# Optimization experiments

Hardware: AMD Instinct MI355X
Metric: run time of the kernel (lower is better)

The kernel has to match this reference:

```python
import jax, jax.numpy as jnp
import numpy as np

N_NODES = 100000
N_EDGES = 1600000
NFEAT, NHID, NCLASS = 128, 64, 40
GN_GROUPS = 32  # min(32, nhid)
GN_EPS = 1e-5
ODE_STEPS = 4   # fixed-step RK4 over t in [0, 1] (stands in for adaptive dopri5)


def setup_inputs() -> dict:
    key = jax.random.key(0)
    ks = jax.random.split(key, 10)
    return {
        "x": jax.random.normal(ks[0], (N_NODES, NFEAT), dtype=jnp.float32),
        "src": jax.random.randint(ks[1], (N_EDGES,), 0, N_NODES),
        "tgt": jax.random.randint(ks[2], (N_EDGES,), 0, N_NODES),
        "mtgt_w": jax.random.uniform(ks[3], (N_EDGES,), dtype=jnp.float32),
        "W0": jax.random.normal(ks[4], (NFEAT, NHID), dtype=jnp.float32) * (1.0 / np.sqrt(NFEAT)),
        "b0": jnp.zeros((NHID,), jnp.float32),
        "gn_w": jnp.ones((NHID,), jnp.float32),
        "gn_b": jnp.zeros((NHID,), jnp.float32),
        "W1": jax.random.normal(ks[5], (NFEAT // 2 + 1, NHID), dtype=jnp.float32) * (1.0 / np.sqrt(NHID + 1)),
        "b1": jnp.zeros((NHID,), jnp.float32),
        "W2": jax.random.normal(ks[6], (NHID, NCLASS), dtype=jnp.float32) * (1.0 / np.sqrt(NHID)),
        "b2": jnp.zeros((NCLASS,), jnp.float32),
    }


def _gconv(h, W, b, src, tgt, mtgt_w, n_nodes):
    # linear transform, gather messages at src, scatter-sum into tgt weighted by Mtgt nonzeros
    s = h @ W + b                                   # [N, out]
    msg = mtgt_w[:, None] * s[src]                  # [E, out]
    return jax.ops.segment_sum(msg, tgt, num_segments=n_nodes)


def _groupnorm(h, gn_w, gn_b):
    n, c = h.shape
    g = h.reshape(n, GN_GROUPS, c // GN_GROUPS)
    mu = g.mean(axis=2, keepdims=True)
    var = g.var(axis=2, keepdims=True)
    g = (g - mu) * jax.lax.rsqrt(var + GN_EPS)
    return g.reshape(n, c) * gn_w + gn_b


def reference(x, src, tgt, mtgt_w, W0, b0, gn_w, gn_b, W1, b1, W2, b2):
    n = x.shape[0]
    # layer 0: GraphConvolution + relu (dropout is identity in eval mode)
    h = jax.nn.relu(_gconv(x, W0, b0, src, tgt, mtgt_w, n))

    # ODE block: dh/dt = relu(gconv(concat([t, groupnorm(h)], 1)))
    def f(t, h):
        hn = _groupnorm(h, gn_w, gn_b)
        tt = jnp.full((n, 1), t, dtype=h.dtype)
        return jax.nn.relu(_gconv(jnp.concatenate([tt, hn], axis=1), W1, b1, src, tgt, mtgt_w, n))

    dt = jnp.float32(1.0 / ODE_STEPS)
    ts = jnp.arange(ODE_STEPS, dtype=jnp.float32) * dt

    def rk4_step(h, t):
        k1 = f(t, h)
        k2 = f(t + dt / 2, h + dt / 2 * k1)
        k3 = f(t + dt / 2, h + dt / 2 * k2)
        k4 = f(t + dt, h + dt * k3)
        return h + dt / 6 * (k1 + 2 * k2 + 2 * k3 + k4), None

    h, _ = jax.lax.scan(rk4_step, h, ts)

    # final GraphConvolution + log_softmax
    out = _gconv(h, W2, b2, src, tgt, mtgt_w, n)
    return jax.nn.log_softmax(out, axis=1)
```

## Files before the change

kernel.cpp:

```cpp
#include <hip/hip_runtime.h>
#include <hip/hip_fp16.h>
#include <math.h>


constexpr int kN = 100000;
constexpr int kE = 1600000;
constexpr int kNPAD = 100352;
constexpr float kDT = 0.25f;
constexpr float kEPS = 1e-5f;

__device__ __forceinline__ float4 ld4(const float* p) { return *(const float4*)p; }
__device__ __forceinline__ void st4(float* p, float4 v) { *(float4*)p = v; }

__global__ void k_zero(int* cnt) {
  int i = blockIdx.x * 256 + threadIdx.x;
  if (i < kN) cnt[i] = 0;
}

__global__ void k_hist(const int* __restrict__ tgt, int* __restrict__ cnt) {
  int e = blockIdx.x * 256 + threadIdx.x;
  if (e < kE) atomicAdd(&cnt[tgt[e]], 1);
}

__global__ __launch_bounds__(256) void k_scan_a(const int* __restrict__ cnt,
                                                int* __restrict__ ptr,
                                                int* __restrict__ bsum) {
  int tid = threadIdx.x;
  int base = blockIdx.x * 1024;
  int i0 = base + tid * 4;
  int v[4];
#pragma unroll
  for (int t = 0; t < 4; ++t) v[t] = (i0 + t < kN) ? cnt[i0 + t] : 0;
  int ts = v[0] + v[1] + v[2] + v[3];
  int lane = tid & 63;
  int x = ts;
#pragma unroll
  for (int off = 1; off < 64; off <<= 1) {
    int y = __shfl_up(x, off);
    if (lane >= off) x += y;
  }
  __shared__ int wsum[4];
  if (lane == 63) wsum[tid >> 6] = x;
  __syncthreads();
  int woff = 0;
#pragma unroll
  for (int w = 0; w < 4; ++w)
    if (w < (tid >> 6)) woff += wsum[w];
  int o = woff + (x - ts);
#pragma unroll
  for (int t = 0; t < 4; ++t) {
    if (i0 + t < kN) ptr[i0 + t] = o;
    o += v[t];
  }
  if (tid == 255) bsum[blockIdx.x] = woff + x;
}

__global__ void k_scan_b(int* bsum, int nb) {
  int lane = threadIdx.x;
  int carry = 0;
  for (int b = 0; b < nb; b += 64) {
    int i = b + lane;
    int v = (i < nb) ? bsum[i] : 0;
    int x = v;
#pragma unroll
    for (int off = 1; off < 64; off <<= 1) {
      int y = __shfl_up(x, off);
      if (lane >= off) x += y;
    }
    if (i < nb) bsum[i] = carry + x - v;
    carry += __shfl(x, 63);
  }
}

__global__ void k_scan_c(const int* __restrict__ bsum, int* __restrict__ ptr,
                         int* __restrict__ runp) {
  int i = blockIdx.x * 256 + threadIdx.x;
  if (i < kN) {
    int v = ptr[i] + bsum[i >> 10];
    ptr[i] = v;
    runp[i] = v;
  }
  if (i == 0) ptr[kN] = kE;
}

__global__ void k_scatter(const int* __restrict__ src, const int* __restrict__ tgt,
                          const float* __restrict__ w, int* __restrict__ runp,
                          float2* __restrict__ meta) {
  int e = blockIdx.x * 256 + threadIdx.x;
  if (e < kE) {
    int t = tgt[e];
    int pos = atomicAdd(&runp[t], 1);
    meta[pos] = make_float2(__int_as_float(src[e]), w[e]);
  }
}

template <bool DSUM>
__device__ __forceinline__ void g_chunk4(const float2* __restrict__ meta,
                                         const float4* __restrict__ S4,
                                         int e, int rem, int slot, int fc,
                                         float4& acc, float& ds) {
  float2 m0 = meta[e + 0], m1 = meta[e + 1], m2 = meta[e + 2], m3 = meta[e + 3];
  int idx = slot == 1 ? __float_as_int(m1.x)
          : slot == 2 ? __float_as_int(m2.x)
          : slot == 3 ? __float_as_int(m3.x)
                      : __float_as_int(m0.x);
  float w = slot == 1 ? m1.y : slot == 2 ? m2.y : slot == 3 ? m3.y : m0.y;
  if (rem < 4) {
    bool ok = slot < rem;
    idx = ok ? idx : 0;
    w = ok ? w : 0.f;
  }
  float4 v = S4[idx * 16 + fc];
  acc.x += w * v.x; acc.y += w * v.y; acc.z += w * v.z; acc.w += w * v.w;
  if (DSUM) ds += w;
}

template <bool DSUM>
__device__ __forceinline__ float4 gather_row4(const float2* __restrict__ meta,
                                              const float4* __restrict__ S4,
                                              int e0, int e1, int slot, int fc,
                                              float& dsum) {
  float4 acc = make_float4(0.f, 0.f, 0.f, 0.f);
  float ds = 0.f;
  int e = e0;
  for (; e + 16 <= e1; e += 16) {
    g_chunk4<DSUM>(meta, S4, e + 0, 4, slot, fc, acc, ds);
    g_chunk4<DSUM>(meta, S4, e + 4, 4, slot, fc, acc, ds);
    g_chunk4<DSUM>(meta, S4, e + 8, 4, slot, fc, acc, ds);
    g_chunk4<DSUM>(meta, S4, e + 12, 4, slot, fc, acc, ds);
  }
  if (e + 8 <= e1) {
    g_chunk4<DSUM>(meta, S4, e + 0, 4, slot, fc, acc, ds);
    g_chunk4<DSUM>(meta, S4, e + 4, 4, slot, fc, acc, ds);
    e += 8;
  }
  if (e + 4 <= e1) {
    g_chunk4<DSUM>(meta, S4, e, 4, slot, fc, acc, ds);
    e += 4;
  }
  if (e < e1) g_chunk4<DSUM>(meta, S4, e, e1 - e, slot, fc, acc, ds);
  acc.x += __shfl_xor(acc.x, 16); acc.y += __shfl_xor(acc.y, 16);
  acc.z += __shfl_xor(acc.z, 16); acc.w += __shfl_xor(acc.w, 16);
  acc.x += __shfl_xor(acc.x, 32); acc.y += __shfl_xor(acc.y, 32);
  acc.z += __shfl_xor(acc.z, 32); acc.w += __shfl_xor(acc.w, 32);
  if (DSUM) {
    ds += __shfl_xor(ds, 16);
    ds += __shfl_xor(ds, 32);
    dsum = ds;
  }
  return acc;
}

__device__ __forceinline__ void g_chunk4h(const float2* __restrict__ meta,
                                          const uint2* __restrict__ Sh,
                                          int e, int rem, int slot, int fc,
                                          float4& acc) {
  float2 m0 = meta[e + 0], m1 = meta[e + 1], m2 = meta[e + 2], m3 = meta[e + 3];
  int idx = slot == 1 ? __float_as_int(m1.x)
          : slot == 2 ? __float_as_int(m2.x)
          : slot == 3 ? __float_as_int(m3.x)
                      : __float_as_int(m0.x);
  float w = slot == 1 ? m1.y : slot == 2 ? m2.y : slot == 3 ? m3.y : m0.y;
  if (rem < 4) {
    bool ok = slot < rem;
    idx = ok ? idx : 0;
    w = ok ? w : 0.f;
  }
  uint2 u = Sh[idx * 16 + fc];
  float2 f01 = __half22float2(*(const __half2*)&u.x);
  float2 f23 = __half22float2(*(const __half2*)&u.y);
  acc.x += w * f01.x; acc.y += w * f01.y;
  acc.z += w * f23.x; acc.w += w * f23.y;
}

__device__ __forceinline__ float4 gather_row4h(const float2* __restrict__ meta,
                                               const uint2* __restrict__ Sh,
                                               int e0, int e1, int slot, int fc) {
  float4 acc = make_float4(0.f, 0.f, 0.f, 0.f);
  int e = e0;
  for (; e + 16 <= e1; e += 16) {
    g_chunk4h(meta, Sh, e + 0, 4, slot, fc, acc);
    g_chunk4h(meta, Sh, e + 4, 4, slot, fc, acc);
    g_chunk4h(meta, Sh, e + 8, 4, slot, fc, acc);
    g_chunk4h(meta, Sh, e + 12, 4, slot, fc, acc);
  }
  if (e + 8 <= e1) {
    g_chunk4h(meta, Sh, e + 0, 4, slot, fc, acc);
    g_chunk4h(meta, Sh, e + 4, 4, slot, fc, acc);
    e += 8;
  }
  if (e + 4 <= e1) {
    g_chunk4h(meta, Sh, e, 4, slot, fc, acc);
    e += 4;
  }
  if (e < e1) g_chunk4h(meta, Sh, e, e1 - e, slot, fc, acc);
  acc.x += __shfl_xor(acc.x, 16); acc.y += __shfl_xor(acc.y, 16);
  acc.z += __shfl_xor(acc.z, 16); acc.w += __shfl_xor(acc.w, 16);
  acc.x += __shfl_xor(acc.x, 32); acc.y += __shfl_xor(acc.y, 32);
  acc.z += __shfl_xor(acc.z, 32); acc.w += __shfl_xor(acc.w, 32);
  return acc;
}

__device__ __forceinline__ void st_half4(unsigned short* p, float4 v) {
  __half2 a = __floats2half2_rn(v.x, v.y);
  __half2 b = __floats2half2_rn(v.z, v.w);
  uint2 u = make_uint2(*(unsigned*)&a, *(unsigned*)&b);
  *(uint2*)p = u;
}

__global__ __launch_bounds__(256) void k_spmm_l0(
    const int* __restrict__ ptr, const float2* __restrict__ meta,
    const float4* __restrict__ S4, float* __restrict__ h,
    unsigned short* __restrict__ hn, const float* __restrict__ gn_w,
    const float* __restrict__ gn_b, float* __restrict__ degw) {
  int wid = (blockIdx.x * 256 + threadIdx.x) >> 6;
  int lane = threadIdx.x & 63;
  if (wid >= kN) return;
  int slot = lane >> 4, fc = lane & 15;
  int e0 = __builtin_amdgcn_readfirstlane(ptr[wid]);
  int e1 = __builtin_amdgcn_readfirstlane(ptr[wid + 1]);
  float dsum = 0.f;
  float4 acc = gather_row4<true>(meta, S4, e0, e1, slot, fc, dsum);
  float4 hv = make_float4(fmaxf(acc.x, 0.f), fmaxf(acc.y, 0.f),
                          fmaxf(acc.z, 0.f), fmaxf(acc.w, 0.f));
  float dx = 0.5f * (hv.x - hv.y);
  float rx = dx * rsqrtf(dx * dx + kEPS);
  float dz = 0.5f * (hv.z - hv.w);
  float rz = dz * rsqrtf(dz * dz + kEPS);
  float4 gw = ld4(gn_w + fc * 4);
  float4 gb = ld4(gn_b + fc * 4);
  float4 o = make_float4(rx * gw.x + gb.x, -rx * gw.y + gb.y,
                         rz * gw.z + gb.z, -rz * gw.w + gb.w);
  if (slot == 0) {
    st4(h + wid * 64 + fc * 4, hv);
    st_half4(hn + wid * 64 + fc * 4, o);
    if (fc == 0) degw[wid] = dsum;
  }
}

__global__ __launch_bounds__(256) void k_spmm_ode(
    const int* __restrict__ ptr, const float2* __restrict__ meta,
    const uint2* __restrict__ Sh, float4* __restrict__ z4) {
  int wid = (blockIdx.x * 256 + threadIdx.x) >> 6;
  int lane = threadIdx.x & 63;
  if (wid >= kN) return;
  int slot = lane >> 4, fc = lane & 15;
  int e0 = __builtin_amdgcn_readfirstlane(ptr[wid]);
  int e1 = __builtin_amdgcn_readfirstlane(ptr[wid + 1]);
  float4 acc = gather_row4h(meta, Sh, e0, e1, slot, fc);
  if (slot == 0) z4[wid * 16 + fc] = acc;
}

__global__ __launch_bounds__(256) void k_gemm_stage(
    const float* __restrict__ z, const float* __restrict__ W1,
    const float* __restrict__ b1, const float* __restrict__ gn_w,
    const float* __restrict__ gn_b, const float* __restrict__ degw,
    float* __restrict__ h, float* __restrict__ kacc,
    unsigned short* __restrict__ hn, float t_s, float a_next, float coef,
    int init_acc, int is_stage3) {
  constexpr int NT = 128, ST = NT + 4, K = 64;
  __shared__ float Wl[K * 64];
  __shared__ float Zt[K * ST];
  const int tid = threadIdx.x;
  const int base = blockIdx.x * NT;
  const float* Wr = W1 + 64;
  for (int i = tid; i < K * 64; i += 256) Wl[i] = Wr[i];
  for (int idx = tid; idx < (K / 4) * NT; idx += 256) {
    int node = idx & (NT - 1);
    int k4 = idx >> 7;
    int g = base + node;
    float4 v = make_float4(0.f, 0.f, 0.f, 0.f);
    if (g < kN) v = ld4(z + (long)g * 64 + k4 * 4);
    int kk = k4 * 4;
    Zt[(kk + 0) * ST + node] = v.x;
    Zt[(kk + 1) * ST + node] = v.y;
    Zt[(kk + 2) * ST + node] = v.z;
    Zt[(kk + 3) * ST + node] = v.w;
  }
  __syncthreads();
  const int c0 = (tid & 15) * 4;
  const int n0 = (tid >> 4) * 8;
  float acc[8][4] = {};
#pragma unroll 8
  for (int j = 0; j < K; ++j) {
    float4 wv = ld4(Wl + j * 64 + c0);
    float4 za = ld4(Zt + j * ST + n0);
    float4 zb = ld4(Zt + j * ST + n0 + 4);
    float zv[8] = {za.x, za.y, za.z, za.w, zb.x, zb.y, zb.z, zb.w};
#pragma unroll
    for (int i = 0; i < 8; ++i) {
      acc[i][0] += zv[i] * wv.x;
      acc[i][1] += zv[i] * wv.y;
      acc[i][2] += zv[i] * wv.z;
      acc[i][3] += zv[i] * wv.w;
    }
  }
  float4 w0r = ld4(W1 + c0);
  float4 b1v = ld4(b1 + c0);
  float4 bias = make_float4(t_s * w0r.x + b1v.x, t_s * w0r.y + b1v.y,
                            t_s * w0r.z + b1v.z, t_s * w0r.w + b1v.w);
  float4 gw = ld4(gn_w + c0);
  float4 gb = ld4(gn_b + c0);
  const float c6 = kDT / 6.f;
#pragma unroll
  for (int i = 0; i < 8; ++i) {
    int g = base + n0 + i;
    if (g >= kN) break;
    float dg = degw[g];
    float4 kv = make_float4(fmaxf(acc[i][0] + dg * bias.x, 0.f),
                            fmaxf(acc[i][1] + dg * bias.y, 0.f),
                            fmaxf(acc[i][2] + dg * bias.z, 0.f),
                            fmaxf(acc[i][3] + dg * bias.w, 0.f));
    long o64 = (long)g * 64 + c0;
    float4 ka;
    if (init_acc) {
      ka = kv;
    } else {
      ka = ld4(kacc + o64);
      ka.x += coef * kv.x; ka.y += coef * kv.y;
      ka.z += coef * kv.z; ka.w += coef * kv.w;
    }
    if (!is_stage3) st4(kacc + o64, ka);
    float4 hv = ld4(h + o64);
    float4 y;
    if (is_stage3) {
      y = make_float4(hv.x + c6 * ka.x, hv.y + c6 * ka.y,
                      hv.z + c6 * ka.z, hv.w + c6 * ka.w);
      st4(h + o64, y);
    } else {
      y = make_float4(hv.x + a_next * kv.x, hv.y + a_next * kv.y,
                      hv.z + a_next * kv.z, hv.w + a_next * kv.w);
    }
    float dx = 0.5f * (y.x - y.y);
    float rx = dx * rsqrtf(dx * dx + kEPS);
    float dz = 0.5f * (y.z - y.w);
    float rz = dz * rsqrtf(dz * dz + kEPS);
    float4 o = make_float4(rx * gw.x + gb.x, -rx * gw.y + gb.y,
                           rz * gw.z + gb.z, -rz * gw.w + gb.w);
    st_half4(hn + o64, o);
  }
}

__global__ __launch_bounds__(256) void k_final(const int* __restrict__ ptr,
                                               const float2* __restrict__ meta,
                                               const float4* __restrict__ s2,
                                               float* __restrict__ out) {
  int wid = (blockIdx.x * 256 + threadIdx.x) >> 6;
  int lane = threadIdx.x & 63;
  if (wid >= kN) return;
  int slot = lane >> 4, fc = lane & 15;
  int e0 = __builtin_amdgcn_readfirstlane(ptr[wid]);
  int e1 = __builtin_amdgcn_readfirstlane(ptr[wid + 1]);
  float dum;
  float4 a = gather_row4<false>(meta, s2, e0, e1, slot, fc, dum);
  bool valid = fc < 10;
  float m = valid ? fmaxf(fmaxf(a.x, a.y), fmaxf(a.z, a.w)) : -INFINITY;
#pragma unroll
  for (int off = 1; off < 16; off <<= 1) m = fmaxf(m, __shfl_xor(m, off));
  float s = valid ? expf(a.x - m) + expf(a.y - m) + expf(a.z - m) + expf(a.w - m)
                  : 0.f;
#pragma unroll
  for (int off = 1; off < 16; off <<= 1) s += __shfl_xor(s, off);
  float lse = logf(s) + m;
  if (slot == 0 && valid)
    st4(out + (long)wid * 40 + fc * 4,
        make_float4(a.x - lse, a.y - lse, a.z - lse, a.w - lse));
}

template <int NCOL, int OST>
__global__ __launch_bounds__(256) void k_gemm64(const float* __restrict__ in,
                                                int in_stride,
                                                const float* __restrict__ W,
                                                const float* __restrict__ bias,
                                                float* __restrict__ out, int beta) {
  constexpr int NT = 128, ST = NT + 4, K = 64;
  __shared__ float Wl[K * 64];
  __shared__ float Zt[K * ST];
  const int tid = threadIdx.x;
  const int base = blockIdx.x * NT;
  for (int i = tid; i < K * 64; i += 256) {
    int j = i >> 6, c = i & 63;
    Wl[i] = (c < NCOL) ? W[j * NCOL + c] : 0.f;
  }
  for (int idx = tid; idx < (K / 4) * NT; idx += 256) {
    int node = idx & (NT - 1);
    int k4 = idx >> 7;
    int g = base + node;
    float4 v = make_float4(0.f, 0.f, 0.f, 0.f);
    if (g < kN) v = ld4(in + (long)g * in_stride + k4 * 4);
    int kk = k4 * 4;
    Zt[(kk + 0) * ST + node] = v.x;
    Zt[(kk + 1) * ST + node] = v.y;
    Zt[(kk + 2) * ST + node] = v.z;
    Zt[(kk + 3) * ST + node] = v.w;
  }
  __syncthreads();
  const int c0 = (tid & 15) * 4;
  const int n0 = (tid >> 4) * 8;
  float acc[8][4] = {};
#pragma unroll 8
  for (int j = 0; j < K; ++j) {
    float4 wv = ld4(Wl + j * 64 + c0);
    float4 za = ld4(Zt + j * ST + n0);
    float4 zb = ld4(Zt + j * ST + n0 + 4);
    float zv[8] = {za.x, za.y, za.z, za.w, zb.x, zb.y, zb.z, zb.w};
#pragma unroll
    for (int i = 0; i < 8; ++i) {
      acc[i][0] += zv[i] * wv.x;
      acc[i][1] += zv[i] * wv.y;
      acc[i][2] += zv[i] * wv.z;
      acc[i][3] += zv[i] * wv.w;
    }
  }
  float4 bv = make_float4(0.f, 0.f, 0.f, 0.f);
  if (bias && c0 < NCOL) bv = ld4(bias + c0);
#pragma unroll
  for (int i = 0; i < 8; ++i) {
    int g = base + n0 + i;
    if (g >= kN) break;
    float* op = out + (long)g * OST + c0;
    float4 o = make_float4(acc[i][0] + bv.x, acc[i][1] + bv.y,
                           acc[i][2] + bv.z, acc[i][3] + bv.w);
    if (beta) {
      float4 p = ld4(op);
      o.x += p.x; o.y += p.y; o.z += p.z; o.w += p.w;
    }
    st4(op, o);
  }
}

extern "C" void kernel_launch(void* const* d_in, const int* in_sizes, int n_in,
                              void* d_out, int out_size, void* d_ws, size_t ws_size,
                              hipStream_t stream) {
  const float* x = (const float*)d_in[0];
  const int* src = (const int*)d_in[1];
  const int* tgt = (const int*)d_in[2];
  const float* mw = (const float*)d_in[3];
  const float* W0 = (const float*)d_in[4];
  const float* b0 = (const float*)d_in[5];
  const float* gnw = (const float*)d_in[6];
  const float* gnb = (const float*)d_in[7];
  const float* W1 = (const float*)d_in[8];
  const float* b1 = (const float*)d_in[9];
  const float* W2 = (const float*)d_in[10];
  const float* b2 = (const float*)d_in[11];
  float* out = (float*)d_out;

  int* cnt_run = (int*)d_ws;
  int* csr_ptr = cnt_run + kNPAD;
  int* bsum = csr_ptr + kNPAD;
  float2* meta = (float2*)(bsum + 128);
  float* degw = (float*)(meta + kE);
  float* h = degw + kNPAD;
  unsigned short* hn = (unsigned short*)(h + (long)kN * 64);
  float* z = (float*)(hn + (long)kN * 64);
  float* kacc = z + (long)kN * 64;

  k_zero<<<391, 256, 0, stream>>>(cnt_run);
  k_hist<<<6250, 256, 0, stream>>>(tgt, cnt_run);
  k_scan_a<<<98, 256, 0, stream>>>(cnt_run, csr_ptr, bsum);
  k_scan_b<<<1, 64, 0, stream>>>(bsum, 98);
  k_scan_c<<<391, 256, 0, stream>>>(bsum, csr_ptr, cnt_run);
  k_scatter<<<6250, 256, 0, stream>>>(src, tgt, mw, cnt_run, meta);

  k_gemm64<64, 64><<<782, 256, 0, stream>>>(x, 128, W0, nullptr, z, 0);
  k_gemm64<64, 64><<<782, 256, 0, stream>>>(x + 64, 128, W0 + 64 * 64, b0, z, 1);
  k_spmm_l0<<<25000, 256, 0, stream>>>(csr_ptr, meta, (const float4*)z, h, hn,
                                       gnw, gnb, degw);

  for (int step = 0; step < 4; ++step) {
    float t = step * kDT;
    const float ts[4] = {t, t + 0.5f * kDT, t + 0.5f * kDT, t + kDT};
    const float an[4] = {0.5f * kDT, 0.5f * kDT, kDT, 0.f};
    const float cf[4] = {1.f, 2.f, 2.f, 1.f};
    for (int s = 0; s < 4; ++s) {
      k_spmm_ode<<<25000, 256, 0, stream>>>(csr_ptr, meta, (const uint2*)hn,
                                            (float4*)z);
      k_gemm_stage<<<782, 256, 0, stream>>>(z, W1, b1, gnw, gnb, degw, h, kacc,
                                            hn, ts[s], an[s], cf[s],
                                            (s == 0) ? 1 : 0, (s == 3) ? 1 : 0);
    }
  }

  k_gemm64<40, 64><<<782, 256, 0, stream>>>(h, 64, W2, b2, z, 0);
  k_final<<<25000, 256, 0, stream>>>(csr_ptr, meta, (const float4*)z, out);
}
```

Measured before the change: 1.830 ms.

## Fuse ODE-stage SpMM with dense transform and ping-pong normalized features

Merges the per-stage sparse gather kernel and the following 64x64 dense transform plus RK4 update into one kernel. Each wave gathers four node rows into shared memory, multiplies them by W1 held in shared memory, and reduces the partial sums with cross-lane shuffles. Two half-precision hn buffers alternate between stages so a stage can read the old features while writing the new ones. The final layer becomes aggregate-then-transform, which removes the z intermediate round trip and a kernel launch. In exchange, each block reloads the full weight matrix into shared memory, and the per-wave GEMM uses scalar FMAs with a shuffle reduction.

Result: faster. 1.484 ms (-19.0%).

```diff
diff --git a/kernel.cpp b/kernel.cpp
--- a/kernel.cpp
+++ b/kernel.cpp
@@ -238,122 +238,165 @@
   }
 }
 
-__global__ __launch_bounds__(256) void k_spmm_ode(
+template <int INIT, int IS3>
+__global__ __launch_bounds__(256) void k_stage_fused(
     const int* __restrict__ ptr, const float2* __restrict__ meta,
-    const uint2* __restrict__ Sh, float4* __restrict__ z4) {
-  int wid = (blockIdx.x * 256 + threadIdx.x) >> 6;
-  int lane = threadIdx.x & 63;
-  if (wid >= kN) return;
-  int slot = lane >> 4, fc = lane & 15;
-  int e0 = __builtin_amdgcn_readfirstlane(ptr[wid]);
-  int e1 = __builtin_amdgcn_readfirstlane(ptr[wid + 1]);
-  float4 acc = gather_row4h(meta, Sh, e0, e1, slot, fc);
-  if (slot == 0) z4[wid * 16 + fc] = acc;
-}
-
-__global__ __launch_bounds__(256) void k_gemm_stage(
-    const float* __restrict__ z, const float* __restrict__ W1,
+    const uint2* __restrict__ hn_in, const float* __restrict__ W1,
     const float* __restrict__ b1, const float* __restrict__ gn_w,
     const float* __restrict__ gn_b, const float* __restrict__ degw,
     float* __restrict__ h, float* __restrict__ kacc,
-    unsigned short* __restrict__ hn, float t_s, float a_next, float coef,
-    int init_acc, int is_stage3) {
-  constexpr int NT = 128, ST = NT + 4, K = 64;
-  __shared__ float Wl[K * 64];
-  __shared__ float Zt[K * ST];
+    unsigned short* __restrict__ hn_out, float t_s, float a_next, float coef) {
+  __shared__ float Wl[64 * 64];
+  __shared__ float zsh[4][4 * 64];
   const int tid = threadIdx.x;
-  const int base = blockIdx.x * NT;
-  const float* Wr = W1 + 64;
-  for (int i = tid; i < K * 64; i += 256) Wl[i] = Wr[i];
-  for (int idx = tid; idx < (K / 4) * NT; idx += 256) {
-    int node = idx & (NT - 1);
-    int k4 = idx >> 7;
-    int g = base + node;
-    float4 v = make_float4(0.f, 0.f, 0.f, 0.f);
-    if (g < kN) v = ld4(z + (long)g * 64 + k4 * 4);
-    int kk = k4 * 4;
-    Zt[(kk + 0) * ST + node] = v.x;
-    Zt[(kk + 1) * ST + node] = v.y;
-    Zt[(kk + 2) * ST + node] = v.z;
-    Zt[(kk + 3) * ST + node] = v.w;
-  }
+  for (int i = tid * 4; i < 4096; i += 1024) *(float4*)&Wl[i] = ld4(W1 + 64 + i);
   __syncthreads();
-  const int c0 = (tid & 15) * 4;
-  const int n0 = (tid >> 4) * 8;
-  float acc[8][4] = {};
-#pragma unroll 8
-  for (int j = 0; j < K; ++j) {
-    float4 wv = ld4(Wl + j * 64 + c0);
-    float4 za = ld4(Zt + j * ST + n0);
-    float4 zb = ld4(Zt + j * ST + n0 + 4);
-    float zv[8] = {za.x, za.y, za.z, za.w, zb.x, zb.y, zb.z, zb.w};
-#pragma unroll
-    for (int i = 0; i < 8; ++i) {
-      acc[i][0] += zv[i] * wv.x;
-      acc[i][1] += zv[i] * wv.y;
-      acc[i][2] += zv[i] * wv.z;
-      acc[i][3] += zv[i] * wv.w;
-    }
-  }
+  const int wave = tid >> 6, lane = tid & 63;
+  const int slot = lane >> 4, fc = lane & 15;
+  const int c0 = fc * 4;
+  const int base = (blockIdx.x * 4 + wave) * 4;
+
   float4 w0r = ld4(W1 + c0);
   float4 b1v = ld4(b1 + c0);
   float4 bias = make_float4(t_s * w0r.x + b1v.x, t_s * w0r.y + b1v.y,
                             t_s * w0r.z + b1v.z, t_s * w0r.w + b1v.w);
   float4 gw = ld4(gn_w + c0);
   float4 gb = ld4(gn_b + c0);
-  const float c6 = kDT / 6.f;
-#pragma unroll
-  for (int i = 0; i < 8; ++i) {
-    int g = base + n0 + i;
-    if (g >= kN) break;
-    float dg = degw[g];
-    float4 kv = make_float4(fmaxf(acc[i][0] + dg * bias.x, 0.f),
-                            fmaxf(acc[i][1] + dg * bias.y, 0.f),
-                            fmaxf(acc[i][2] + dg * bias.z, 0.f),
-                            fmaxf(acc[i][3] + dg * bias.w, 0.f));
-    long o64 = (long)g * 64 + c0;
-    float4 ka;
-    if (init_acc) {
-      ka = kv;
-    } else {
-      ka = ld4(kacc + o64);
-      ka.x += coef * kv.x; ka.y += coef * kv.y;
-      ka.z += coef * kv.z; ka.w += coef * kv.w;
-    }
-    if (!is_stage3) st4(kacc + o64, ka);
-    float4 hv = ld4(h + o64);
-    float4 y;
-    if (is_stage3) {
-      y = make_float4(hv.x + c6 * ka.x, hv.y + c6 * ka.y,
-                      hv.z + c6 * ka.z, hv.w + c6 * ka.w);
-      st4(h + o64, y);
-    } else {
-      y = make_float4(hv.x + a_next * kv.x, hv.y + a_next * kv.y,
-                      hv.z + a_next * kv.z, hv.w + a_next * kv.w);
-    }
-    float dx = 0.5f * (y.x - y.y);
-    float rx = dx * rsqrtf(dx * dx + kEPS);
-    float dz = 0.5f * (y.z - y.w);
-    float rz = dz * rsqrtf(dz * dz + kEPS);
-    float4 o = make_float4(rx * gw.x + gb.x, -rx * gw.y + gb.y,
-                           rz * gw.z + gb.z, -rz * gw.w + gb.w);
-    st_half4(hn + o64, o);
-  }
-}
-
-__global__ __launch_bounds__(256) void k_final(const int* __restrict__ ptr,
-                                               const float2* __restrict__ meta,
-                                               const float4* __restrict__ s2,
-                                               float* __restrict__ out) {
-  int wid = (blockIdx.x * 256 + threadIdx.x) >> 6;
-  int lane = threadIdx.x & 63;
-  if (wid >= kN) return;
-  int slot = lane >> 4, fc = lane & 15;
-  int e0 = __builtin_amdgcn_readfirstlane(ptr[wid]);
-  int e1 = __builtin_amdgcn_readfirstlane(ptr[wid + 1]);
+
+#pragma unroll
+  for (int u = 0; u < 4; ++u) {
+    int n = base + u;
+    int e0 = __builtin_amdgcn_readfirstlane(ptr[n]);
+    int e1 = __builtin_amdgcn_readfirstlane(ptr[n + 1]);
+    float4 a = gather_row4h(meta, hn_in, e0, e1, slot, fc);
+    if (slot == 0) st4(&zsh[wave][u * 64 + c0], a);
+  }
+
+  float4 a0 = make_float4(0, 0, 0, 0), a1 = a0, a2 = a0, a3 = a0;
+#pragma unroll
+  for (int t = 0; t < 16; ++t) {
+    int j = slot * 16 + t;
+    float4 w4 = ld4(&Wl[j * 64 + c0]);
+    float z0 = zsh[wave][0 * 64 + j];
+    float z1 = zsh[wave][1 * 64 + j];
+    float z2 = zsh[wave][2 * 64 + j];
+    float z3 = zsh[wave][3 * 64 + j];
+    a0.x += z0 * w4.x; a0.y += z0 * w4.y; a0.z += z0 * w4.z; a0.w += z0 * w4.w;
+    a1.x += z1 * w4.x; a1.y += z1 * w4.y; a1.z += z1 * w4.z; a1.w += z1 * w4.w;
+    a2.x += z2 * w4.x; a2.y += z2 * w4.y; a2.z += z2 * w4.z; a2.w += z2 * w4.w;
+    a3.x += z3 * w4.x; a3.y += z3 * w4.y; a3.z += z3 * w4.z; a3.w += z3 * w4.w;
+  }
+#pragma unroll
+  for (int off = 16; off <= 32; off <<= 1) {
+    a0.x += __shfl_xor(a0.x, off); a0.y += __shfl_xor(a0.y, off);
+    a0.z += __shfl_xor(a0.z, off); a0.w += __shfl_xor(a0.w, off);
+    a1.x += __shfl_xor(a1.x, off); a1.y += __shfl_xor(a1.y, off);
+    a1.z += __shfl_xor(a1.z, off); a1.w += __shfl_xor(a1.w, off);
+    a2.x += __shfl_xor(a2.x, off); a2.y += __shfl_xor(a2.y, off);
+    a2.z += __shfl_xor(a2.z, off); a2.w += __shfl_xor(a2.w, off);
+    a3.x += __shfl_xor(a3.x, off); a3.y += __shfl_xor(a3.y, off);
+    a3.z += __shfl_xor(a3.z, off); a3.w += __shfl_xor(a3.w, off);
+  }
+
+  const int n = base + slot;
+  float4 accs;
+  accs.x = slot == 0 ? a0.x : slot == 1 ? a1.x : slot == 2 ? a2.x : a3.x;
+  accs.y = slot == 0 ? a0.y : slot == 1 ? a1.y : slot == 2 ? a2.y : a3.y;
+  accs.z = slot == 0 ? a0.z : slot == 1 ? a1.z : slot == 2 ? a2.z : a3.z;
+  accs.w = slot == 0 ? a0.w : slot == 1 ? a1.w : slot == 2 ? a2.w : a3.w;
+  float dg = degw[n];
+  float4 kv = make_float4(fmaxf(accs.x + dg * bias.x, 0.f),
+                          fmaxf(accs.y + dg * bias.y, 0.f),
+                          fmaxf(accs.z + dg * bias.z, 0.f),
+                          fmaxf(accs.w + dg * bias.w, 0.f));
+  long o = (long)n * 64 + c0;
+  float4 ka;
+  if (INIT) {
+    ka = kv;
+  } else {
+    ka = ld4(kacc + o);
+    ka.x += coef * kv.x; ka.y += coef * kv.y;
+    ka.z += coef * kv.z; ka.w += coef * kv.w;
+  }
+  if (!IS3) st4(kacc + o, ka);
+  float4 hv = ld4(h + o);
+  float4 y;
+  if (IS3) {
+    const float c6 = kDT / 6.f;
+    y = make_float4(hv.x + c6 * ka.x, hv.y + c6 * ka.y,
+                    hv.z + c6 * ka.z, hv.w + c6 * ka.w);
+    st4(h + o, y);
+  } else {
+    y = make_float4(hv.x + a_next * kv.x, hv.y + a_next * kv.y,
+                    hv.z + a_next * kv.z, hv.w + a_next * kv.w);
+  }
+  float dx = 0.5f * (y.x - y.y);
+  float rx = dx * rsqrtf(dx * dx + kEPS);
+  float dz = 0.5f * (y.z - y.w);
+  float rz = dz * rsqrtf(dz * dz + kEPS);
+  float4 on = make_float4(rx * gw.x + gb.x, -rx * gw.y + gb.y,
+                          rz * gw.z + gb.z, -rz * gw.w + gb.w);
+  st_half4(hn_out + o, on);
+}
+
+__global__ __launch_bounds__(256) void k_fin2(
+    const int* __restrict__ ptr, const float2* __restrict__ meta,
+    const float4* __restrict__ h4, const float* __restrict__ W2,
+    const float* __restrict__ b2, const float* __restrict__ degw,
+    float* __restrict__ out) {
+  __shared__ float Wl[64 * 40];
+  __shared__ float zsh[4][4 * 64];
+  const int tid = threadIdx.x;
+  for (int i = tid; i < 2560; i += 256) Wl[i] = W2[i];
+  __syncthreads();
+  const int wave = tid >> 6, lane = tid & 63;
+  const int slot = lane >> 4, fc = lane & 15;
+  const int c0 = fc * 4;
+  const bool valid = fc < 10;
+  const int base = (blockIdx.x * 4 + wave) * 4;
   float dum;
-  float4 a = gather_row4<false>(meta, s2, e0, e1, slot, fc, dum);
-  bool valid = fc < 10;
+#pragma unroll
+  for (int u = 0; u < 4; ++u) {
+    int n = base + u;
+    int e0 = __builtin_amdgcn_readfirstlane(ptr[n]);
+    int e1 = __builtin_amdgcn_readfirstlane(ptr[n + 1]);
+    float4 a = gather_row4<false>(meta, h4, e0, e1, slot, fc, dum);
+    if (slot == 0) st4(&zsh[wave][u * 64 + c0], a);
+  }
+  float4 a0 = make_float4(0, 0, 0, 0), a1 = a0, a2 = a0, a3 = a0;
+#pragma unroll
+  for (int t = 0; t < 16; ++t) {
+    int j = slot * 16 + t;
+    float4 w4 = valid ? ld4(&Wl[j * 40 + c0]) : make_float4(0, 0, 0, 0);
+    float z0 = zsh[wave][0 * 64 + j];
+    float z1 = zsh[wave][1 * 64 + j];
+    float z2 = zsh[wave][2 * 64 + j];
+    float z3 = zsh[wave][3 * 64 + j];
+    a0.x += z0 * w4.x; a0.y += z0 * w4.y; a0.z += z0 * w4.z; a0.w += z0 * w4.w;
+    a1.x += z1 * w4.x; a1.y += z1 * w4.y; a1.z += z1 * w4.z; a1.w += z1 * w4.w;
+    a2.x += z2 * w4.x; a2.y += z2 * w4.y; a2.z += z2 * w4.z; a2.w += z2 * w4.w;
+    a3.x += z3 * w4.x; a3.y += z3 * w4.y; a3.z += z3 * w4.z; a3.w += z3 * w4.w;
+  }
+#pragma unroll
+  for (int off = 16; off <= 32; off <<= 1) {
+    a0.x += __shfl_xor(a0.x, off); a0.y += __shfl_xor(a0.y, off);
+    a0.z += __shfl_xor(a0.z, off); a0.w += __shfl_xor(a0.w, off);
+    a1.x += __shfl_xor(a1.x, off); a1.y += __shfl_xor(a1.y, off);
+    a1.z += __shfl_xor(a1.z, off); a1.w += __shfl_xor(a1.w, off);
+    a2.x += __shfl_xor(a2.x, off); a2.y += __shfl_xor(a2.y, off);
+    a2.z += __shfl_xor(a2.z, off); a2.w += __shfl_xor(a2.w, off);
+    a3.x += __shfl_xor(a3.x, off); a3.y += __shfl_xor(a3.y, off);
+    a3.z += __shfl_xor(a3.z, off); a3.w += __shfl_xor(a3.w, off);
+  }
+  const int n = base + slot;
+  float4 a;
+  a.x = slot == 0 ? a0.x : slot == 1 ? a1.x : slot == 2 ? a2.x : a3.x;
+  a.y = slot == 0 ? a0.y : slot == 1 ? a1.y : slot == 2 ? a2.y : a3.y;
+  a.z = slot == 0 ? a0.z : slot == 1 ? a1.z : slot == 2 ? a2.z : a3.z;
+  a.w = slot == 0 ? a0.w : slot == 1 ? a1.w : slot == 2 ? a2.w : a3.w;
+  float dg = degw[n];
+  float4 b2v = valid ? ld4(b2 + c0) : make_float4(0, 0, 0, 0);
+  a.x += dg * b2v.x; a.y += dg * b2v.y; a.z += dg * b2v.z; a.w += dg * b2v.w;
   float m = valid ? fmaxf(fmaxf(a.x, a.y), fmaxf(a.z, a.w)) : -INFINITY;
 #pragma unroll
   for (int off = 1; off < 16; off <<= 1) m = fmaxf(m, __shfl_xor(m, off));
@@ -362,8 +405,8 @@
 #pragma unroll
   for (int off = 1; off < 16; off <<= 1) s += __shfl_xor(s, off);
   float lse = logf(s) + m;
-  if (slot == 0 && valid)
-    st4(out + (long)wid * 40 + fc * 4,
+  if (valid)
+    st4(out + (long)n * 40 + c0,
         make_float4(a.x - lse, a.y - lse, a.z - lse, a.w - lse));
 }
 
@@ -452,8 +495,9 @@
   float2* meta = (float2*)(bsum + 128);
   float* degw = (float*)(meta + kE);
   float* h = degw + kNPAD;
-  unsigned short* hn = (unsigned short*)(h + (long)kN * 64);
-  float* z = (float*)(hn + (long)kN * 64);
+  unsigned short* hnA = (unsigned short*)(h + (long)kN * 64);
+  unsigned short* hnB = hnA + (long)kN * 64;
+  float* z = (float*)(hnB + (long)kN * 64);
   float* kacc = z + (long)kN * 64;
 
   k_zero<<<391, 256, 0, stream>>>(cnt_run);
@@ -465,23 +509,25 @@
 
   k_gemm64<64, 64><<<782, 256, 0, stream>>>(x, 128, W0, nullptr, z, 0);
   k_gemm64<64, 64><<<782, 256, 0, stream>>>(x + 64, 128, W0 + 64 * 64, b0, z, 1);
-  k_spmm_l0<<<25000, 256, 0, stream>>>(csr_ptr, meta, (const float4*)z, h, hn,
+  k_spmm_l0<<<25000, 256, 0, stream>>>(csr_ptr, meta, (const float4*)z, h, hnA,
                                        gnw, gnb, degw);
 
   for (int step = 0; step < 4; ++step) {
     float t = step * kDT;
-    const float ts[4] = {t, t + 0.5f * kDT, t + 0.5f * kDT, t + kDT};
-    const float an[4] = {0.5f * kDT, 0.5f * kDT, kDT, 0.f};
-    const float cf[4] = {1.f, 2.f, 2.f, 1.f};
-    for (int s = 0; s < 4; ++s) {
-      k_spmm_ode<<<25000, 256, 0, stream>>>(csr_ptr, meta, (const uint2*)hn,
-                                            (float4*)z);
-      k_gemm_stage<<<782, 256, 0, stream>>>(z, W1, b1, gnw, gnb, degw, h, kacc,
-                                            hn, ts[s], an[s], cf[s],
-                                            (s == 0) ? 1 : 0, (s == 3) ? 1 : 0);
-    }
-  }
-
-  k_gemm64<40, 64><<<782, 256, 0, stream>>>(h, 64, W2, b2, z, 0);
-  k_final<<<25000, 256, 0, stream>>>(csr_ptr, meta, (const float4*)z, out);
-}
+    k_stage_fused<1, 0><<<6250, 256, 0, stream>>>(
+        csr_ptr, meta, (const uint2*)hnA, W1, b1, gnw, gnb, degw, h, kacc, hnB,
+        t, 0.5f * kDT, 1.f);
+    k_stage_fused<0, 0><<<6250, 256, 0, stream>>>(
+        csr_ptr, meta, (const uint2*)hnB, W1, b1, gnw, gnb, degw, h, kacc, hnA,
+        t + 0.5f * kDT, 0.5f * kDT, 2.f);
+    k_stage_fused<0, 0><<<6250, 256, 0, stream>>>(
+        csr_ptr, meta, (const uint2*)hnA, W1, b1, gnw, gnb, degw, h, kacc, hnB,
+        t + 0.5f * kDT, kDT, 2.f);
+    k_stage_fused<0, 1><<<6250, 256, 0, stream>>>(
+        csr_ptr, meta, (const uint2*)hnB, W1, b1, gnw, gnb, degw, h, kacc, hnA,
+        t + kDT, 0.f, 1.f);
+  }
+
+  k_fin2<<<6250, 256, 0, stream>>>(csr_ptr, meta, (const float4*)h, W2, b2,
+                                   degw, out);
+}
```
